# Optimization experiments

Measured on AMD Instinct MI355X. Metric: run time of the kernel, lower is better.

## Reference

```python
import jax, jax.numpy as jnp
import numpy as np

D_MODEL = 768
N_HEADS = 12
HEAD_DIM = D_MODEL // N_HEADS


def setup_inputs() -> dict:
    key = jax.random.key(0)
    ks = jax.random.split(key, 9)
    s = 1.0 / np.sqrt(D_MODEL)
    inp = {
        "inputs": jax.random.normal(ks[0], (1, 4096, D_MODEL), dtype=jnp.float32),
        "Wq": jax.random.uniform(ks[1], (D_MODEL, D_MODEL), jnp.float32, -s, s),
        "bq": jax.random.uniform(ks[2], (D_MODEL,), jnp.float32, -s, s),
        "Wk": jax.random.uniform(ks[3], (D_MODEL, D_MODEL), jnp.float32, -s, s),
        "bk": jax.random.uniform(ks[4], (D_MODEL,), jnp.float32, -s, s),
        "Wv": jax.random.uniform(ks[5], (D_MODEL, D_MODEL), jnp.float32, -s, s),
        "bv": jax.random.uniform(ks[6], (D_MODEL,), jnp.float32, -s, s),
        "Wo": jax.random.uniform(ks[7], (D_MODEL, D_MODEL), jnp.float32, -s, s),
        "bo": jax.random.uniform(ks[8], (D_MODEL,), jnp.float32, -s, s),
    }
    return inp


def reference(inputs, Wq, bq, Wk, bk, Wv, bv, Wo, bo):
    B, S, D = inputs.shape
    H, Hd = N_HEADS, HEAD_DIM

    def split_heads(x):  # [B,S,D] -> [B,H,S,Hd]
        return x.reshape(B, S, H, Hd).transpose(0, 2, 1, 3)

    # nn.Linear computes x @ W.T + b
    Q = split_heads(inputs @ Wq.T + bq)
    K = split_heads(inputs @ Wk.T + bk)
    V = split_heads(inputs @ Wv.T + bv)

    scores = jnp.einsum("bhsd,bhtd->bhst", Q, K) / jnp.sqrt(jnp.float32(Hd))
    causal = jnp.tril(jnp.ones((S, S), dtype=bool))  # True = keep
    scores = jnp.where(causal, scores, -jnp.inf)
    attn = jax.nn.softmax(scores, axis=-1)  # dropout is identity in eval

    out = jnp.einsum("bhst,bhtd->bhsd", attn, V)
    out = out.transpose(0, 2, 1, 3).reshape(B, S, D)
    return out @ Wo.T + bo
```

## Files before the change

### kernel.cpp

```cpp
#include <hip/hip_runtime.h>
#include <stdint.h>

#define SEQ 4096
#define DM 768
#define NH 12
#define HD 64

typedef unsigned short u16;
typedef short short8 __attribute__((ext_vector_type(8)));
typedef float floatx4 __attribute__((ext_vector_type(4)));
typedef u16 u16x4 __attribute__((ext_vector_type(4)));

__device__ inline u16 f2b(float f) {
  union { float f; uint32_t u; } v; v.f = f;
  uint32_t u = v.u;
  return (u16)((u + 0x7fffu + ((u >> 16) & 1u)) >> 16);
}

__device__ inline float b2f(u16 x) {
  union { uint32_t u; float f; } v; v.u = ((uint32_t)x) << 16;
  return v.f;
}

#if defined(__has_builtin)
#if __has_builtin(__builtin_amdgcn_cvt_pk_bf16_f32)
#define HAVE_PK_BF16 1
#endif
#endif

__device__ inline uint32_t pk_bf16(float a, float b) {
#ifdef HAVE_PK_BF16
  typedef __bf16 bf16x2_t __attribute__((ext_vector_type(2)));
  union { bf16x2_t v; uint32_t u; } c;
  c.v = __builtin_amdgcn_cvt_pk_bf16_f32(a, b);
  return c.u;
#else
  return (uint32_t)f2b(a) | ((uint32_t)f2b(b) << 16);
#endif
}

__device__ inline void load_lds16(const void* g, void* l) {
  __builtin_amdgcn_global_load_lds(
      (const __attribute__((address_space(1))) uint32_t*)g,
      (__attribute__((address_space(3))) uint32_t*)l, 16, 0, 0);
}

__global__ __launch_bounds__(256) void convert_all(
    const float* __restrict__ X, const float* __restrict__ Wq,
    const float* __restrict__ Wk, const float* __restrict__ Wv,
    const float* __restrict__ Wo,
    u16* __restrict__ Xb, u16* __restrict__ Wqb, u16* __restrict__ Wkb,
    u16* __restrict__ Wvb, u16* __restrict__ Wob) {
  int t = blockIdx.x * 256 + threadIdx.x;
  const int NX = SEQ * DM / 4;
  const int NW = DM * DM / 4;
  const float* src; u16* dst; int off;
  if (t < NX)               { src = X;  dst = Xb;  off = t; }
  else if (t < NX + NW)     { src = Wq; dst = Wqb; off = t - NX; }
  else if (t < NX + 2 * NW) { src = Wk; dst = Wkb; off = t - NX - NW; }
  else if (t < NX + 3 * NW) { src = Wv; dst = Wvb; off = t - NX - 2 * NW; }
  else if (t < NX + 4 * NW) { src = Wo; dst = Wob; off = t - NX - 3 * NW; }
  else return;
  float4 v = *(const float4*)(src + (size_t)off * 4);
  uint2 o;
  o.x = pk_bf16(v.x, v.y);
  o.y = pk_bf16(v.z, v.w);
  *(uint2*)(dst + (size_t)off * 4) = o;
}

__global__ __launch_bounds__(256) void gemm_qkv(
    const u16* __restrict__ Xb,
    const u16* __restrict__ Wqb, const u16* __restrict__ Wkb,
    const u16* __restrict__ Wvb,
    const float* __restrict__ bq, const float* __restrict__ bk,
    const float* __restrict__ bv,
    u16* __restrict__ Qh, u16* __restrict__ Kh, u16* __restrict__ VtG) {
  const u16* W; const float* bias;
  const int z = blockIdx.z;
  if (z == 0)      { W = Wqb; bias = bq; }
  else if (z == 1) { W = Wkb; bias = bk; }
  else             { W = Wvb; bias = bv; }

  __shared__ u16 smem[16384];

  const int tid = threadIdx.x;
  const int wave = tid >> 6, lane = tid & 63;
  const int g = lane >> 4, ln = lane & 15;
  const int m0 = blockIdx.y * 64, n0 = blockIdx.x * 64;
  const int wm = (wave & 1) * 32, wn = (wave >> 1) * 32;
  const int srow = lane >> 3;
  const int schunk = (lane & 7) ^ srow;
  const int swz = ln & 7;

  floatx4 acc[2][2] = {};

#pragma unroll
  for (int i = 0; i < 2; ++i) {
    int u = wave * 2 + i;
    load_lds16(Xb + (size_t)(m0 + u * 8 + srow) * DM + schunk * 8, smem + u * 512);
    load_lds16(W + (size_t)(n0 + u * 8 + srow) * DM + schunk * 8,
               smem + 8192 + u * 512);
  }

  for (int kt = 0; kt < 12; ++kt) {
    const int cur = kt & 1;
    __syncthreads();
    if (kt < 11) {
      const int k0 = (kt + 1) * 64, nb = cur ^ 1;
#pragma unroll
      for (int i = 0; i < 2; ++i) {
        int u = wave * 2 + i;
        load_lds16(Xb + (size_t)(m0 + u * 8 + srow) * DM + k0 + schunk * 8,
                   smem + nb * 4096 + u * 512);
        load_lds16(W + (size_t)(n0 + u * 8 + srow) * DM + k0 + schunk * 8,
                   smem + 8192 + nb * 4096 + u * 512);
      }
    }
    const u16* Ac = smem + cur * 4096;
    const u16* Bc = smem + 8192 + cur * 4096;
    short8 af[2][2], bf[2][2];
#pragma unroll
    for (int mi = 0; mi < 2; ++mi)
#pragma unroll
      for (int kh = 0; kh < 2; ++kh)
        af[mi][kh] = *(const short8*)(Ac + (wm + mi * 16 + ln) * 64 +
                                      ((kh * 4 + g) ^ swz) * 8);
#pragma unroll
    for (int ni = 0; ni < 2; ++ni)
#pragma unroll
      for (int kh = 0; kh < 2; ++kh)
        bf[ni][kh] = *(const short8*)(Bc + (wn + ni * 16 + ln) * 64 +
                                      ((kh * 4 + g) ^ swz) * 8);
#pragma unroll
    for (int kh = 0; kh < 2; ++kh)
#pragma unroll
      for (int mi = 0; mi < 2; ++mi)
#pragma unroll
        for (int ni = 0; ni < 2; ++ni)
          acc[mi][ni] = __builtin_amdgcn_mfma_f32_16x16x32_bf16(
              af[mi][kh], bf[ni][kh], acc[mi][ni], 0, 0, 0);
  }

  const float qscale = 0.125f * 1.44269504089f;
  const int hh = n0 >> 6;
  __syncthreads();

  if (z == 2) {
#pragma unroll
    for (int mi = 0; mi < 2; ++mi) {
      int row0 = wm + mi * 16 + g * 4;
#pragma unroll
      for (int ni = 0; ni < 2; ++ni) {
        int col = wn + ni * 16 + ln;
        float b = bias[n0 + col];
        uint2 o;
        o.x = pk_bf16(acc[mi][ni][0] + b, acc[mi][ni][1] + b);
        o.y = pk_bf16(acc[mi][ni][2] + b, acc[mi][ni][3] + b);
        *(uint2*)(smem + col * 72 + row0) = o;
      }
    }
    __syncthreads();
#pragma unroll
    for (int t = 0; t < 2; ++t) {
      int unit = tid + t * 256;
      int dcol = unit >> 3, ch = unit & 7;
      short8 v = *(const short8*)(smem + dcol * 72 + ch * 8);
      *(short8*)(VtG + ((size_t)(hh * 64 + dcol)) * SEQ + m0 + ch * 8) = v;
    }
  } else {
    u16* out = (z == 0) ? Qh : Kh;
    float cs = (z == 0) ? qscale : 1.0f;
#pragma unroll
    for (int mi = 0; mi < 2; ++mi) {
      int row0 = wm + mi * 16 + g * 4;
#pragma unroll
      for (int ni = 0; ni < 2; ++ni) {
        int col = wn + ni * 16 + ln;
        float b = bias[n0 + col];
        uint32_t w0 = pk_bf16((acc[mi][ni][0] + b) * cs, (acc[mi][ni][1] + b) * cs);
        uint32_t w1 = pk_bf16((acc[mi][ni][2] + b) * cs, (acc[mi][ni][3] + b) * cs);
        smem[(row0 + 0) * 72 + col] = (u16)w0;
        smem[(row0 + 1) * 72 + col] = (u16)(w0 >> 16);
        smem[(row0 + 2) * 72 + col] = (u16)w1;
        smem[(row0 + 3) * 72 + col] = (u16)(w1 >> 16);
      }
    }
    __syncthreads();
#pragma unroll
    for (int t = 0; t < 2; ++t) {
      int unit = tid + t * 256;
      int row = unit >> 3, ch = unit & 7;
      short8 v = *(const short8*)(smem + row * 72 + ch * 8);
      *(short8*)(out + ((size_t)hh * SEQ + m0 + row) * HD + ch * 8) = v;
    }
  }
}

#define CHUNK 16
#define M0 40.0f
__global__ __launch_bounds__(512, 6) void attn_chunk(
    const u16* __restrict__ Qh, const u16* __restrict__ Kh,
    const u16* __restrict__ VtG, u16* __restrict__ Opart,
    float2* __restrict__ Mlp) {
  const int h = blockIdx.x;
  const int b = 79 - blockIdx.y;
  int qB, ci;
  if (b < 8)       { qB = b;               ci = 0; }
  else if (b < 24) { int r = b - 8;  qB = 8 + (r >> 1); ci = r & 1; }
  else if (b < 48) { int r = b - 24; int d = r / 3; qB = 16 + d; ci = r - d * 3; }
  else             { int r = b - 48; qB = 24 + (r >> 2); ci = r & 3; }
  const int kb0 = ci * CHUNK;
  const int kb1 = min(kb0 + CHUNK, 2 * qB + 2);

  const int tid = threadIdx.x, wave = tid >> 6, lane = tid & 63;
  const int g = lane >> 4, ln = lane & 15;
  const int q0 = qB * 128;
  const int qwave = q0 + wave * 16;
  const int srow = lane >> 3;
  const int schunk = (lane & 7) ^ srow;
  const int swz = ln & 7;

  __shared__ u16 Ks[2 * 4096];
  __shared__ u16 Vt[2 * 4096];
  __shared__ u16 Ps[8][16 * 72];

  const int qglob = qwave + ln;
  const u16* Qbase = Qh + ((size_t)h * SEQ + qglob) * HD;
  short8 aq[2] = { *(const short8*)(Qbase + g * 8),
                   *(const short8*)(Qbase + 32 + g * 8) };

  floatx4 oacc[4] = {};
  floatx4 lacc = {};
  u16* PsW = &Ps[wave][0];

  const size_t kbase = (size_t)h * SEQ * HD;
  const size_t vbase = (size_t)h * 64 * SEQ;

  load_lds16(Kh + kbase + (size_t)(kb0 * 64 + wave * 8 + srow) * HD + schunk * 8,
             Ks + wave * 512);
  load_lds16(VtG + vbase + (size_t)(wave * 8 + srow) * SEQ + kb0 * 64 + schunk * 8,
             Vt + wave * 512);

  for (int kb = kb0; kb < kb1; ++kb) {
    const int cur = (kb - kb0) & 1;
    __syncthreads();
    if (kb + 1 < kb1) {
      const int nb = cur ^ 1, kn = (kb + 1) * 64;
      load_lds16(Kh + kbase + (size_t)(kn + wave * 8 + srow) * HD + schunk * 8,
                 Ks + nb * 4096 + wave * 512);
      load_lds16(VtG + vbase + (size_t)(wave * 8 + srow) * SEQ + kn + schunk * 8,
                 Vt + nb * 4096 + wave * 512);
    }
    const u16* Kc = Ks + cur * 4096;
    const u16* Vc = Vt + cur * 4096;

    if (kb * 64 > qwave + 15) continue;

    floatx4 st[4] = {};
#pragma unroll
    for (int kh = 0; kh < 2; ++kh)
#pragma unroll
      for (int nt = 0; nt < 4; ++nt) {
        short8 kf = *(const short8*)(Kc + (nt * 16 + ln) * 64 +
                                     ((kh * 4 + g) ^ swz) * 8);
        st[nt] = __builtin_amdgcn_mfma_f32_16x16x32_bf16(kf, aq[kh], st[nt], 0, 0, 0);
      }

    if (kb * 64 + 63 > qwave) {
#pragma unroll
      for (int nt = 0; nt < 4; ++nt)
#pragma unroll
        for (int r = 0; r < 4; ++r)
          if (kb * 64 + nt * 16 + g * 4 + r > qglob) st[nt][r] = -1e30f;
    }

#pragma unroll
    for (int nt = 0; nt < 4; ++nt) {
#pragma unroll
      for (int r = 0; r < 4; ++r)
        st[nt][r] = __builtin_amdgcn_exp2f(st[nt][r] - M0);
      lacc += st[nt];
    }

#pragma unroll
    for (int nt = 0; nt < 4; ++nt) {
      uint2 pk;
      pk.x = pk_bf16(st[nt][0], st[nt][1]);
      pk.y = pk_bf16(st[nt][2], st[nt][3]);
      *(uint2*)(PsW + ln * 72 + nt * 16 + g * 4) = pk;
    }

#pragma unroll
    for (int ks = 0; ks < 2; ++ks) {
      short8 ap = *(const short8*)(PsW + ln * 72 + ks * 32 + g * 8);
#pragma unroll
      for (int nt = 0; nt < 4; ++nt) {
        short8 vf = *(const short8*)(Vc + (nt * 16 + ln) * 64 +
                                     ((ks * 4 + g) ^ swz) * 8);
        oacc[nt] = __builtin_amdgcn_mfma_f32_16x16x32_bf16(vf, ap, oacc[nt], 0, 0, 0);
      }
    }
  }

  float l_i = lacc[0] + lacc[1] + lacc[2] + lacc[3];
  l_i += __shfl_xor(l_i, 16);
  l_i += __shfl_xor(l_i, 32);

  const int slot = (h * 32 + qB) * 4 + ci;
  float inv = 1.f / l_i;
  int qloc = wave * 16 + ln;
  u16* Op = Opart + (size_t)slot * 8192 + qloc * 64;
#pragma unroll
  for (int nt = 0; nt < 4; ++nt) {
    uint2 o;
    o.x = pk_bf16(oacc[nt][0] * inv, oacc[nt][1] * inv);
    o.y = pk_bf16(oacc[nt][2] * inv, oacc[nt][3] * inv);
    *(uint2*)(Op + nt * 16 + g * 4) = o;
  }
  if (g == 0) Mlp[(size_t)slot * 128 + qloc] = make_float2(M0, l_i);
}

__global__ __launch_bounds__(256) void attn_merge(
    const u16* __restrict__ Opart, const float2* __restrict__ Mlp,
    u16* __restrict__ Ob) {
  const int h = blockIdx.x, qB = blockIdx.y;
  const int n = (qB >> 3) + 1;
  const int base = (h * 32 + qB) * 4;
  const int q = threadIdx.x >> 1;
  const int d0 = (threadIdx.x & 1) * 32;

  float m[4], l[4];
  float M = -1e30f;
  for (int i = 0; i < n; ++i) {
    float2 ml = Mlp[(size_t)(base + i) * 128 + q];
    m[i] = ml.x; l[i] = ml.y;
    M = fmaxf(M, m[i]);
  }
  float w[4], L = 0.f;
  for (int i = 0; i < n; ++i) {
    w[i] = l[i] * __builtin_amdgcn_exp2f(m[i] - M);
    L += w[i];
  }
  float invL = 1.f / L;

  float acc[32];
#pragma unroll
  for (int j = 0; j < 32; ++j) acc[j] = 0.f;
  for (int i = 0; i < n; ++i) {
    float wi = w[i] * invL;
    const u16* src = Opart + (size_t)(base + i) * 8192 + q * 64 + d0;
#pragma unroll
    for (int c = 0; c < 4; ++c) {
      short8 a = ((const short8*)src)[c];
#pragma unroll
      for (int j = 0; j < 8; ++j) acc[c * 8 + j] += wi * b2f((u16)a[j]);
    }
  }

  u16* dst = Ob + (size_t)(qB * 128 + q) * DM + h * HD + d0;
#pragma unroll
  for (int c = 0; c < 4; ++c) {
    uint4 o;
    o.x = pk_bf16(acc[c * 8 + 0], acc[c * 8 + 1]);
    o.y = pk_bf16(acc[c * 8 + 2], acc[c * 8 + 3]);
    o.z = pk_bf16(acc[c * 8 + 4], acc[c * 8 + 5]);
    o.w = pk_bf16(acc[c * 8 + 6], acc[c * 8 + 7]);
    ((uint4*)dst)[c] = o;
  }
}

__global__ __launch_bounds__(256) void gemm_out(
    const u16* __restrict__ Ab, const u16* __restrict__ Wob,
    const float* __restrict__ bo, float* __restrict__ Cout) {
  __shared__ u16 smem[16384];

  const int tid = threadIdx.x;
  const int wave = tid >> 6, lane = tid & 63;
  const int g = lane >> 4, ln = lane & 15;
  const int m0 = blockIdx.y * 64, n0 = blockIdx.x * 64;
  const int wm = (wave & 1) * 32, wn = (wave >> 1) * 32;
  const int srow = lane >> 3;
  const int schunk = (lane & 7) ^ srow;
  const int swz = ln & 7;

  floatx4 acc[2][2] = {};

#pragma unroll
  for (int i = 0; i < 2; ++i) {
    int u = wave * 2 + i;
    load_lds16(Ab + (size_t)(m0 + u * 8 + srow) * DM + schunk * 8, smem + u * 512);
    load_lds16(Wob + (size_t)(n0 + u * 8 + srow) * DM + schunk * 8,
               smem + 8192 + u * 512);
  }

  for (int kt = 0; kt < 12; ++kt) {
    const int cur = kt & 1;
    __syncthreads();
    if (kt < 11) {
      const int k0 = (kt + 1) * 64, nb = cur ^ 1;
#pragma unroll
      for (int i = 0; i < 2; ++i) {
        int u = wave * 2 + i;
        load_lds16(Ab + (size_t)(m0 + u * 8 + srow) * DM + k0 + schunk * 8,
                   smem + nb * 4096 + u * 512);
        load_lds16(Wob + (size_t)(n0 + u * 8 + srow) * DM + k0 + schunk * 8,
                   smem + 8192 + nb * 4096 + u * 512);
      }
    }
    const u16* Ac = smem + cur * 4096;
    const u16* Bc = smem + 8192 + cur * 4096;
    short8 af[2][2], bf[2][2];
#pragma unroll
    for (int mi = 0; mi < 2; ++mi)
#pragma unroll
      for (int kh = 0; kh < 2; ++kh)
        af[mi][kh] = *(const short8*)(Ac + (wm + mi * 16 + ln) * 64 +
                                      ((kh * 4 + g) ^ swz) * 8);
#pragma unroll
    for (int ni = 0; ni < 2; ++ni)
#pragma unroll
      for (int kh = 0; kh < 2; ++kh)
        bf[ni][kh] = *(const short8*)(Bc + (wn + ni * 16 + ln) * 64 +
                                      ((kh * 4 + g) ^ swz) * 8);
#pragma unroll
    for (int kh = 0; kh < 2; ++kh)
#pragma unroll
      for (int mi = 0; mi < 2; ++mi)
#pragma unroll
        for (int ni = 0; ni < 2; ++ni)
          acc[mi][ni] = __builtin_amdgcn_mfma_f32_16x16x32_bf16(
              af[mi][kh], bf[ni][kh], acc[mi][ni], 0, 0, 0);
  }

#pragma unroll
  for (int mi = 0; mi < 2; ++mi) {
    int row = m0 + wm + mi * 16 + g * 4;
#pragma unroll
    for (int ni = 0; ni < 2; ++ni) {
      int col = n0 + wn + ni * 16 + ln;
      float b = bo[col];
#pragma unroll
      for (int r = 0; r < 4; ++r)
        Cout[(size_t)(row + r) * DM + col] = acc[mi][ni][r] + b;
    }
  }
}

extern "C" void kernel_launch(void* const* d_in, const int* in_sizes, int n_in,
                              void* d_out, int out_size, void* d_ws, size_t ws_size,
                              hipStream_t stream) {
  const float* X  = (const float*)d_in[0];
  const float* Wq = (const float*)d_in[1];
  const float* bq = (const float*)d_in[2];
  const float* Wk = (const float*)d_in[3];
  const float* bk = (const float*)d_in[4];
  const float* Wv = (const float*)d_in[5];
  const float* bv = (const float*)d_in[6];
  const float* Wo = (const float*)d_in[7];
  const float* bo = (const float*)d_in[8];
  float* out = (float*)d_out;

  char* ws = (char*)d_ws;
  u16* Xb  = (u16*)ws; ws += (size_t)SEQ * DM * 2;
  u16* Wqb = (u16*)ws; ws += (size_t)DM * DM * 2;
  u16* Wkb = (u16*)ws; ws += (size_t)DM * DM * 2;
  u16* Wvb = (u16*)ws; ws += (size_t)DM * DM * 2;
  u16* Wob = (u16*)ws; ws += (size_t)DM * DM * 2;
  u16* Qh  = (u16*)ws; ws += (size_t)NH * SEQ * HD * 2;
  u16* Kh  = (u16*)ws; ws += (size_t)NH * SEQ * HD * 2;
  u16* VtG = (u16*)ws; ws += (size_t)NH * SEQ * HD * 2;
  u16* Ob  = (u16*)ws; ws += (size_t)SEQ * DM * 2;
  u16* Opart = (u16*)ws; ws += (size_t)NH * 32 * 4 * 128 * 64 * 2;
  float2* Mlp = (float2*)ws; ws += (size_t)NH * 32 * 4 * 128 * sizeof(float2);

  convert_all<<<5376, 256, 0, stream>>>(X, Wq, Wk, Wv, Wo, Xb, Wqb, Wkb, Wvb, Wob);

  dim3 gq(DM / 64, SEQ / 64, 3);
  gemm_qkv<<<gq, 256, 0, stream>>>(Xb, Wqb, Wkb, Wvb, bq, bk, bv, Qh, Kh, VtG);

  dim3 ga(NH, 80);
  attn_chunk<<<ga, 512, 0, stream>>>(Qh, Kh, VtG, Opart, Mlp);

  dim3 gm(NH, 32);
  attn_merge<<<gm, 256, 0, stream>>>(Opart, Mlp, Ob);

  dim3 go(DM / 64, SEQ / 64);
  gemm_out<<<go, 256, 0, stream>>>(Ob, Wob, bo, out);
}
```

Before: 186.0 us.

## Switch attention to 32x32x16 MFMA with in-register P transpose via permlane32_swap

The chunked attention kernel now uses 4 waves of 32 query rows each, built on 32x32x16 bf16 MFMAs instead of 8 waves of 16 rows using 16x16x32. The probability tile is repacked in registers with v_permlane32_swap, which drops the per-wave LDS scratch buffer and its store/load round trip before the PV MFMA. Block size falls to 256 threads, so each wave issues more K/V async loads. Register pressure goes up with 16-wide accumulators, and fewer threads per block change occupancy.

Result: faster. 181.2 us (-2.6%).

```diff
diff --git a/kernel.cpp b/kernel.cpp
--- a/kernel.cpp
+++ b/kernel.cpp
@@ -9,6 +9,7 @@
 typedef unsigned short u16;
 typedef short short8 __attribute__((ext_vector_type(8)));
 typedef float floatx4 __attribute__((ext_vector_type(4)));
+typedef float floatx16 __attribute__((ext_vector_type(16)));
 typedef u16 u16x4 __attribute__((ext_vector_type(4)));
 
 __device__ inline u16 f2b(float f) {
@@ -37,6 +38,10 @@
 #else
   return (uint32_t)f2b(a) | ((uint32_t)f2b(b) << 16);
 #endif
+}
+
+__device__ inline void pl32swap(uint32_t& a, uint32_t& b) {
+  asm("v_permlane32_swap_b32 %0, %1" : "+v"(a), "+v"(b));
 }
 
 __device__ inline void load_lds16(const void* g, void* l) {
@@ -198,7 +203,7 @@
 
 #define CHUNK 16
 #define M0 40.0f
-__global__ __launch_bounds__(512, 6) void attn_chunk(
+__global__ __launch_bounds__(256, 4) void attn_chunk(
     const u16* __restrict__ Qh, const u16* __restrict__ Kh,
     const u16* __restrict__ VtG, u16* __restrict__ Opart,
     float2* __restrict__ Mlp) {
@@ -213,111 +218,129 @@
   const int kb1 = min(kb0 + CHUNK, 2 * qB + 2);
 
   const int tid = threadIdx.x, wave = tid >> 6, lane = tid & 63;
-  const int g = lane >> 4, ln = lane & 15;
+  const int hi = lane >> 5, lq = lane & 31;
   const int q0 = qB * 128;
-  const int qwave = q0 + wave * 16;
+  const int qwave = q0 + wave * 32;
   const int srow = lane >> 3;
   const int schunk = (lane & 7) ^ srow;
-  const int swz = ln & 7;
+  const int rsw = lane & 7;
 
   __shared__ u16 Ks[2 * 4096];
   __shared__ u16 Vt[2 * 4096];
-  __shared__ u16 Ps[8][16 * 72];
-
-  const int qglob = qwave + ln;
+
+  const int qglob = qwave + lq;
   const u16* Qbase = Qh + ((size_t)h * SEQ + qglob) * HD;
-  short8 aq[2] = { *(const short8*)(Qbase + g * 8),
-                   *(const short8*)(Qbase + 32 + g * 8) };
-
-  floatx4 oacc[4] = {};
+  short8 aq[4];
+#pragma unroll
+  for (int s = 0; s < 4; ++s)
+    aq[s] = *(const short8*)(Qbase + s * 16 + hi * 8);
+
+  floatx16 oacc[2] = {};
   floatx4 lacc = {};
-  u16* PsW = &Ps[wave][0];
 
   const size_t kbase = (size_t)h * SEQ * HD;
   const size_t vbase = (size_t)h * 64 * SEQ;
 
-  load_lds16(Kh + kbase + (size_t)(kb0 * 64 + wave * 8 + srow) * HD + schunk * 8,
-             Ks + wave * 512);
-  load_lds16(VtG + vbase + (size_t)(wave * 8 + srow) * SEQ + kb0 * 64 + schunk * 8,
-             Vt + wave * 512);
+#pragma unroll
+  for (int i = 0; i < 2; ++i) {
+    int u = wave * 2 + i;
+    load_lds16(Kh + kbase + (size_t)(kb0 * 64 + u * 8 + srow) * HD + schunk * 8,
+               Ks + u * 512);
+    load_lds16(VtG + vbase + (size_t)(u * 8 + srow) * SEQ + kb0 * 64 + schunk * 8,
+               Vt + u * 512);
+  }
 
   for (int kb = kb0; kb < kb1; ++kb) {
     const int cur = (kb - kb0) & 1;
     __syncthreads();
     if (kb + 1 < kb1) {
       const int nb = cur ^ 1, kn = (kb + 1) * 64;
-      load_lds16(Kh + kbase + (size_t)(kn + wave * 8 + srow) * HD + schunk * 8,
-                 Ks + nb * 4096 + wave * 512);
-      load_lds16(VtG + vbase + (size_t)(wave * 8 + srow) * SEQ + kn + schunk * 8,
-                 Vt + nb * 4096 + wave * 512);
+#pragma unroll
+      for (int i = 0; i < 2; ++i) {
+        int u = wave * 2 + i;
+        load_lds16(Kh + kbase + (size_t)(kn + u * 8 + srow) * HD + schunk * 8,
+                   Ks + nb * 4096 + u * 512);
+        load_lds16(VtG + vbase + (size_t)(u * 8 + srow) * SEQ + kn + schunk * 8,
+                   Vt + nb * 4096 + u * 512);
+      }
     }
     const u16* Kc = Ks + cur * 4096;
     const u16* Vc = Vt + cur * 4096;
 
-    if (kb * 64 > qwave + 15) continue;
-
-    floatx4 st[4] = {};
-#pragma unroll
-    for (int kh = 0; kh < 2; ++kh)
-#pragma unroll
-      for (int nt = 0; nt < 4; ++nt) {
-        short8 kf = *(const short8*)(Kc + (nt * 16 + ln) * 64 +
-                                     ((kh * 4 + g) ^ swz) * 8);
-        st[nt] = __builtin_amdgcn_mfma_f32_16x16x32_bf16(kf, aq[kh], st[nt], 0, 0, 0);
+    if (kb * 64 > qwave + 31) continue;
+
+    floatx16 st[2] = {};
+#pragma unroll
+    for (int s = 0; s < 4; ++s)
+#pragma unroll
+      for (int kblk = 0; kblk < 2; ++kblk) {
+        short8 kf = *(const short8*)(Kc + (kblk * 32 + lq) * 64 +
+                                     ((s * 2 + hi) ^ rsw) * 8);
+        st[kblk] = __builtin_amdgcn_mfma_f32_32x32x16_bf16(kf, aq[s], st[kblk],
+                                                           0, 0, 0);
       }
 
     if (kb * 64 + 63 > qwave) {
 #pragma unroll
-      for (int nt = 0; nt < 4; ++nt)
-#pragma unroll
-        for (int r = 0; r < 4; ++r)
-          if (kb * 64 + nt * 16 + g * 4 + r > qglob) st[nt][r] = -1e30f;
-    }
-
-#pragma unroll
-    for (int nt = 0; nt < 4; ++nt) {
+      for (int kblk = 0; kblk < 2; ++kblk)
+#pragma unroll
+        for (int r = 0; r < 16; ++r) {
+          int key = kb * 64 + kblk * 32 + (r & 3) + 8 * (r >> 2) + 4 * hi;
+          if (key > qglob) st[kblk][r] = -1e30f;
+        }
+    }
+
+    uint32_t w[2][8];
+#pragma unroll
+    for (int kblk = 0; kblk < 2; ++kblk) {
+#pragma unroll
+      for (int r = 0; r < 16; ++r)
+        st[kblk][r] = __builtin_amdgcn_exp2f(st[kblk][r] - M0);
 #pragma unroll
       for (int r = 0; r < 4; ++r)
-        st[nt][r] = __builtin_amdgcn_exp2f(st[nt][r] - M0);
-      lacc += st[nt];
-    }
-
-#pragma unroll
-    for (int nt = 0; nt < 4; ++nt) {
-      uint2 pk;
-      pk.x = pk_bf16(st[nt][0], st[nt][1]);
-      pk.y = pk_bf16(st[nt][2], st[nt][3]);
-      *(uint2*)(PsW + ln * 72 + nt * 16 + g * 4) = pk;
-    }
-
-#pragma unroll
-    for (int ks = 0; ks < 2; ++ks) {
-      short8 ap = *(const short8*)(PsW + ln * 72 + ks * 32 + g * 8);
-#pragma unroll
-      for (int nt = 0; nt < 4; ++nt) {
-        short8 vf = *(const short8*)(Vc + (nt * 16 + ln) * 64 +
-                                     ((ks * 4 + g) ^ swz) * 8);
-        oacc[nt] = __builtin_amdgcn_mfma_f32_16x16x32_bf16(vf, ap, oacc[nt], 0, 0, 0);
+        lacc[r] += st[kblk][r] + st[kblk][4 + r] + st[kblk][8 + r] +
+                   st[kblk][12 + r];
+#pragma unroll
+      for (int i = 0; i < 8; ++i)
+        w[kblk][i] = pk_bf16(st[kblk][2 * i], st[kblk][2 * i + 1]);
+    }
+
+#pragma unroll
+    for (int ks = 0; ks < 4; ++ks) {
+      const int kblk = ks >> 1, base = (ks & 1) * 4;
+      uint32_t d0 = w[kblk][base + 0], d2 = w[kblk][base + 2];
+      uint32_t d1 = w[kblk][base + 1], d3 = w[kblk][base + 3];
+      pl32swap(d0, d2);
+      pl32swap(d1, d3);
+      union { uint32_t u[4]; short8 s; } bp;
+      bp.u[0] = d0; bp.u[1] = d1; bp.u[2] = d2; bp.u[3] = d3;
+#pragma unroll
+      for (int dblk = 0; dblk < 2; ++dblk) {
+        short8 vf = *(const short8*)(Vc + (dblk * 32 + lq) * 64 +
+                                     ((ks * 2 + hi) ^ rsw) * 8);
+        oacc[dblk] = __builtin_amdgcn_mfma_f32_32x32x16_bf16(vf, bp.s, oacc[dblk],
+                                                             0, 0, 0);
       }
     }
   }
 
   float l_i = lacc[0] + lacc[1] + lacc[2] + lacc[3];
-  l_i += __shfl_xor(l_i, 16);
   l_i += __shfl_xor(l_i, 32);
 
   const int slot = (h * 32 + qB) * 4 + ci;
   float inv = 1.f / l_i;
-  int qloc = wave * 16 + ln;
+  int qloc = wave * 32 + lq;
   u16* Op = Opart + (size_t)slot * 8192 + qloc * 64;
 #pragma unroll
-  for (int nt = 0; nt < 4; ++nt) {
-    uint2 o;
-    o.x = pk_bf16(oacc[nt][0] * inv, oacc[nt][1] * inv);
-    o.y = pk_bf16(oacc[nt][2] * inv, oacc[nt][3] * inv);
-    *(uint2*)(Op + nt * 16 + g * 4) = o;
-  }
-  if (g == 0) Mlp[(size_t)slot * 128 + qloc] = make_float2(M0, l_i);
+  for (int dblk = 0; dblk < 2; ++dblk)
+#pragma unroll
+    for (int qd = 0; qd < 4; ++qd) {
+      uint2 o;
+      o.x = pk_bf16(oacc[dblk][qd * 4 + 0] * inv, oacc[dblk][qd * 4 + 1] * inv);
+      o.y = pk_bf16(oacc[dblk][qd * 4 + 2] * inv, oacc[dblk][qd * 4 + 3] * inv);
+      *(uint2*)(Op + dblk * 32 + qd * 8 + hi * 4) = o;
+    }
+  if (hi == 0) Mlp[(size_t)slot * 128 + qloc] = make_float2(M0, l_i);
 }
 
 __global__ __launch_bounds__(256) void attn_merge(
@@ -479,7 +502,7 @@
   gemm_qkv<<<gq, 256, 0, stream>>>(Xb, Wqb, Wkb, Wvb, bq, bk, bv, Qh, Kh, VtG);
 
   dim3 ga(NH, 80);
-  attn_chunk<<<ga, 512, 0, stream>>>(Qh, Kh, VtG, Opart, Mlp);
+  attn_chunk<<<ga, 256, 0, stream>>>(Qh, Kh, VtG, Opart, Mlp);
 
   dim3 gm(NH, 32);
   attn_merge<<<gm, 256, 0, stream>>>(Opart, Mlp, Ob);
```
